# Performance work log

Hardware: AMD Instinct MI355X
Metric: run time of the kernel (lower is better)

The kernel has to match this reference:

```python
import jax, jax.numpy as jnp
import numpy as np

N = 50000      # total nodes
E = 500000     # edges
D = 128        # in_channels
B = 50         # graphs in batch
NPG = N // B   # nodes per graph (equal-sized graphs)
RATIO = 0.5
ALPHA = 0.6


def setup_inputs() -> dict:
    key = jax.random.key(0)
    ks = jax.random.split(key, 8)
    x = jax.random.normal(ks[0], (N, D), dtype=jnp.float32)
    edge_index = jax.random.randint(ks[1], (2, E), 0, N, dtype=jnp.int32)
    batch = jnp.repeat(jnp.arange(B, dtype=jnp.int32), NPG)  # sorted, equal blocks
    s = 1.0 / np.sqrt(D)
    # GCNConv(D,1) for structure score
    W_s = jax.random.normal(ks[2], (D, 1), dtype=jnp.float32) * s
    b_s = jnp.zeros((1,), dtype=jnp.float32)
    # Linear(D,1) for feature score
    W_f = jax.random.normal(ks[3], (1, D), dtype=jnp.float32) * s
    b_f = jnp.zeros((1,), dtype=jnp.float32)
    # GCNConv(D,D) fusion layer
    W_fu = jax.random.normal(ks[4], (D, D), dtype=jnp.float32) * s
    b_fu = jnp.zeros((D,), dtype=jnp.float32)
    return {"x": x, "edge_index": edge_index, "batch": batch,
            "W_s": W_s, "b_s": b_s, "W_f": W_f, "b_f": b_f,
            "W_fu": W_fu, "b_fu": b_fu}


def gcn_conv(x, src, dst, W, b, n):
    """PyG GCNConv: add self loops, symmetric D^-1/2 (A+I) D^-1/2 @ (xW) + b."""
    xw = x @ W                                  # [n, out]
    loop = jnp.arange(n, dtype=src.dtype)
    s = jnp.concatenate([src, loop])
    d = jnp.concatenate([dst, loop])
    deg = jax.ops.segment_sum(jnp.ones_like(s, dtype=xw.dtype), d, num_segments=n)
    dinv = jax.lax.rsqrt(jnp.maximum(deg, 1e-12))
    norm = dinv[s] * dinv[d]                    # [E+n]
    out = jax.ops.segment_sum(norm[:, None] * xw[s], d, num_segments=n)
    return out + b


def reference(x, edge_index, batch, W_s, b_s, W_f, b_f, W_fu, b_fu):
    src, dst = edge_index[0], edge_index[1]
    # fused score: alpha * structure (GCN) + (1-alpha) * feature (Linear)
    score_s = gcn_conv(x, src, dst, W_s, b_s, N)[:, 0]          # [N]
    score_f = (x @ W_f.T + b_f)[:, 0]                           # [N]
    score = jnp.tanh(ALPHA * score_s + (1.0 - ALPHA) * score_f)
    # per-graph top-k (equal-sized graphs -> dense [B, NPG] view, like the torch topk)
    k = int(np.ceil(RATIO * NPG))
    dense = score.reshape(B, NPG)
    order = jnp.argsort(-dense, axis=-1)                        # descending
    offsets = (jnp.arange(B, dtype=jnp.int32) * NPG)[:, None]
    perm = (order[:, :k].astype(jnp.int32) + offsets).reshape(-1)  # [B*k]
    # fusion conv on full graph, then gather selected nodes
    x_fused = gcn_conv(x, src, dst, W_fu, b_fu, N)              # [N, D]
    x_ae = x_fused[perm]                                        # [B*k, D]
    x_out = x_ae * score[perm][:, None]                         # multiplier == 1
    batch_out = batch[perm]
    # filter_adj: remap node ids, keep edges with both endpoints selected
    nodemap = jnp.full((N,), -1, dtype=jnp.int32).at[perm].set(
        jnp.arange(perm.shape[0], dtype=jnp.int32))
    r, c = nodemap[src], nodemap[dst]
    m = (r >= 0) & (c >= 0)
    edge_index_new = jnp.stack([r[m], c[m]], axis=0)
    return (x_out, edge_index_new, batch_out, perm, x_ae)
```

## Files before the change

kernel.cpp:

```cpp
#include <hip/hip_runtime.h>
#include <math.h>

#define N_NODES 50000
#define N_EDGES 500000
#define DIM     128
#define NGRAPH  50
#define NPGC    1000
#define KSEL    500
#define SORT_N  1024
#define NBE     489
#define GEMM_BLKS 782
#define EDGE_BLKS 1954
#define NDINV     196
#define GATH_BLKS 6250
#define DEGB    64
#define NCHUNK  1954


__global__ __launch_bounds__(256) void k1b_deg(const int* __restrict__ dst,
                                               int* __restrict__ degpriv,
                                               int* __restrict__ eslot) {
    int t = threadIdx.x;
    int b = blockIdx.x;
    int* priv = degpriv + b * N_NODES;
    for (int c = b; c < NCHUNK; c += 2 * DEGB) {
        int e1 = (c << 8) + t;
        int cB = c + DEGB;
        int e2 = (cB << 8) + t;
        int d1 = (e1 < N_EDGES) ? dst[e1] : -1;
        int d2 = (cB < NCHUNK && e2 < N_EDGES) ? dst[e2] : -1;
        if (d1 >= 0)
            eslot[e1] = __hip_atomic_fetch_add(&priv[d1], 1, __ATOMIC_RELAXED,
                                               __HIP_MEMORY_SCOPE_WORKGROUP);
        if (d2 >= 0)
            eslot[e2] = __hip_atomic_fetch_add(&priv[d2], 1, __ATOMIC_RELAXED,
                                               __HIP_MEMORY_SCOPE_WORKGROUP);
    }
}


__global__ __launch_bounds__(256) void k1a_gemm_dots(const float* __restrict__ x,
                                                     const float* __restrict__ W,
                                                     float* __restrict__ xw,
                                                     const float* __restrict__ Ws,
                                                     const float* __restrict__ Wf,
                                                     const float* __restrict__ bf,
                                                     double* __restrict__ pack,
                                                     double* __restrict__ sf) {
    __shared__ float lds[12544];
    int t = threadIdx.x;
    float* Wt  = lds;
    float* Xt  = lds + 8192;
    float* Wsl = lds + 12288;
    float* Wfl = lds + 12416;
    int cg = t & 15;
    int ng = t >> 4;
    int node_base = blockIdx.x * 64;

    if (t < 128) Wsl[t] = Ws[t];
    else         Wfl[t - 128] = Wf[t - 128];

    int dn  = t >> 2;
    int dk4 = (t & 3) << 4;
    double ps = 0.0, pf = 0.0;

    float4 acc[4][2];
    #pragma unroll
    for (int nn = 0; nn < 4; nn++) {
        acc[nn][0] = make_float4(0.f, 0.f, 0.f, 0.f);
        acc[nn][1] = make_float4(0.f, 0.f, 0.f, 0.f);
    }
    for (int half = 0; half < 2; half++) {
        const float4* Wg = (const float4*)(W + half * 64 * DIM);
        float4* Wl = (float4*)Wt;
        #pragma unroll
        for (int i = 0; i < 8; i++) {
            int f = t + i * 256;
            Wl[f] = Wg[f];
        }
        #pragma unroll
        for (int i = 0; i < 4; i++) {
            int f = t + i * 256;
            int row = f >> 4, col = f & 15;
            int node = node_base + row;
            float4 v = make_float4(0.f, 0.f, 0.f, 0.f);
            if (node < N_NODES) v = *(const float4*)&x[(size_t)node * DIM + half * 64 + col * 4];
            *(float4*)&Xt[(row << 6) + ((col ^ (row & 15)) << 2)] = v;
        }
        __syncthreads();
        #pragma unroll 2
        for (int kc = 0; kc < 16; kc++) {
            int k = kc << 2;
            float4 wa[4], wb[4];
            #pragma unroll
            for (int kk = 0; kk < 4; kk++) {
                wa[kk] = *(const float4*)&Wt[(k + kk) * DIM + (cg << 2)];
                wb[kk] = *(const float4*)&Wt[(k + kk) * DIM + (cg << 2) + 64];
            }
            int csw = (kc ^ ng) << 2;
            #pragma unroll
            for (int nn = 0; nn < 4; nn++) {
                float4 xv = *(const float4*)&Xt[((ng + (nn << 4)) << 6) + csw];
                acc[nn][0].x += xv.x * wa[0].x + xv.y * wa[1].x + xv.z * wa[2].x + xv.w * wa[3].x;
                acc[nn][0].y += xv.x * wa[0].y + xv.y * wa[1].y + xv.z * wa[2].y + xv.w * wa[3].y;
                acc[nn][0].z += xv.x * wa[0].z + xv.y * wa[1].z + xv.z * wa[2].z + xv.w * wa[3].z;
                acc[nn][0].w += xv.x * wa[0].w + xv.y * wa[1].w + xv.z * wa[2].w + xv.w * wa[3].w;
                acc[nn][1].x += xv.x * wb[0].x + xv.y * wb[1].x + xv.z * wb[2].x + xv.w * wb[3].x;
                acc[nn][1].y += xv.x * wb[0].y + xv.y * wb[1].y + xv.z * wb[2].y + xv.w * wb[3].y;
                acc[nn][1].z += xv.x * wb[0].z + xv.y * wb[1].z + xv.z * wb[2].z + xv.w * wb[3].z;
                acc[nn][1].w += xv.x * wb[0].w + xv.y * wb[1].w + xv.z * wb[2].w + xv.w * wb[3].w;
            }
        }
        #pragma unroll 4
        for (int j = 0; j < 16; j++) {
            int k = dk4 + j;
            int col = k >> 2, sub = k & 3;
            double xd = (double)Xt[(dn << 6) + ((col ^ (dn & 15)) << 2) + sub];
            ps += xd * (double)Wsl[half * 64 + k];
            pf += xd * (double)Wfl[half * 64 + k];
        }
        __syncthreads();
    }
    #pragma unroll
    for (int nn = 0; nn < 4; nn++) {
        int node = node_base + ng + (nn << 4);
        if (node < N_NODES) {
            *(float4*)&xw[(size_t)node * DIM + (cg << 2)]      = acc[nn][0];
            *(float4*)&xw[(size_t)node * DIM + (cg << 2) + 64] = acc[nn][1];
        }
    }
    ps += __shfl_down(ps, 2, 64); ps += __shfl_down(ps, 1, 64);
    pf += __shfl_down(pf, 2, 64); pf += __shfl_down(pf, 1, 64);
    if ((t & 3) == 0) {
        int node = node_base + dn;
        if (node < N_NODES) {
            pack[2 * node + 1] = ps;
            sf[node] = pf + (double)bf[0];
        }
    }
}


__global__ __launch_bounds__(256) void k2_merge(int* __restrict__ degpriv,
                                                int* __restrict__ deg,
                                                int* __restrict__ rowoff,
                                                int* __restrict__ bsums256,
                                                double* __restrict__ pack,
                                                float* __restrict__ dinvf) {
    int t = threadIdx.x;
    int lane = t & 63, wid = t >> 6;
    int i = blockIdx.x * 256 + t;
    int o = 0;
    if (i < N_NODES) {
        #pragma unroll 8
        for (int b = 0; b < DEGB; b++) {
            int* p = &degpriv[b * N_NODES + i];
            int c = *p;
            *p = o;
            o += c;
        }
        deg[i] = o;
        double di = 1.0 / sqrt((double)(o + 1));
        pack[2 * i] = di;
        dinvf[i] = (float)di;
    }
    __shared__ int ws4[4];
    int incl = o;
    #pragma unroll
    for (int off = 1; off < 64; off <<= 1) {
        int u = __shfl_up(incl, off, 64);
        if (lane >= off) incl += u;
    }
    if (lane == 63) ws4[wid] = incl;
    __syncthreads();
    int woff = 0;
    #pragma unroll
    for (int w = 0; w < 4; w++) if (w < wid) woff += ws4[w];
    if (i < N_NODES) rowoff[i] = incl - o + woff;
    if (t == 255) bsums256[blockIdx.x] = woff + incl;
}


__global__ __launch_bounds__(256) void k3_csr(const int* __restrict__ src,
                                              const int* __restrict__ dst,
                                              const int* __restrict__ rowoff,
                                              const int* __restrict__ bsums256,
                                              const int* __restrict__ degpriv,
                                              const int* __restrict__ eslot,
                                              int* __restrict__ csr) {
    __shared__ int bsN[256];
    int t = threadIdx.x;
    if (t < 64) {
        int carry = 0;
        #pragma unroll
        for (int ch = 0; ch < 4; ch++) {
            int i = ch * 64 + t;
            int v = (i < NDINV) ? bsums256[i] : 0;
            int incl = v;
            #pragma unroll
            for (int off = 1; off < 64; off <<= 1) {
                int u = __shfl_up(incl, off, 64);
                if (t >= off) incl += u;
            }
            bsN[i] = incl - v + carry;
            carry += __shfl(incl, 63, 64);
        }
    }
    __syncthreads();
    int e = blockIdx.x * 256 + t;
    if (e >= N_EDGES) return;
    int d = dst[e];
    int owner = (e >> 8) & (DEGB - 1);
    int pos = rowoff[d] + bsN[d >> 8] + degpriv[owner * N_NODES + d] + eslot[e];
    csr[pos] = src[e];
}


__global__ __launch_bounds__(256) void k3b_score(const int* __restrict__ csr,
                                                 const int* __restrict__ rowoff,
                                                 const int* __restrict__ bsums256,
                                                 const int* __restrict__ deg,
                                                 const double* __restrict__ pack,
                                                 double* __restrict__ score_sd) {
    __shared__ int bsN[256];
    int t = threadIdx.x;
    if (t < 64) {
        int carry = 0;
        #pragma unroll
        for (int ch = 0; ch < 4; ch++) {
            int i = ch * 64 + t;
            int v = (i < NDINV) ? bsums256[i] : 0;
            int incl = v;
            #pragma unroll
            for (int off = 1; off < 64; off <<= 1) {
                int u = __shfl_up(incl, off, 64);
                if (t >= off) incl += u;
            }
            bsN[i] = incl - v + carry;
            carry += __shfl(incl, 63, 64);
        }
    }
    __syncthreads();
    int node = blockIdx.x * 256 + t;
    if (node >= N_NODES) return;
    int base = rowoff[node] + bsN[node >> 8];
    int cnt  = deg[node];
    double acc0 = 0.0, acc1 = 0.0;
    int i = 0;
    for (; i + 2 <= cnt; i += 2) {
        int s0 = csr[base + i];
        int s1 = csr[base + i + 1];
        double2 p0 = ((const double2*)pack)[s0];
        double2 p1 = ((const double2*)pack)[s1];
        acc0 += p0.x * p0.y;
        acc1 += p1.x * p1.y;
    }
    if (i < cnt) {
        int s0 = csr[base + i];
        double2 p0 = ((const double2*)pack)[s0];
        acc0 += p0.x * p0.y;
    }
    score_sd[node] = pack[2 * node] * (acc0 + acc1);
}


__global__ __launch_bounds__(512) void k4_topk(const double* __restrict__ score_sd,
                                               const double* __restrict__ pack,
                                               const double* __restrict__ sf,
                                               const float* __restrict__ bs,
                                               const int* __restrict__ batch,
                                               int* __restrict__ perm, int* __restrict__ nodemap,
                                               float* __restrict__ scoref_sel,
                                               float* __restrict__ out, long o2, long o3) {
    __shared__ double key[SORT_N];
    __shared__ int    idx[SORT_N];
    int g = blockIdx.x, t = threadIdx.x;
    const double A = 0.6, OMA = 1.0 - 0.6;
    double bsv = (double)bs[0];
    for (int i = t; i < SORT_N; i += 512) {
        if (i < NPGC) {
            int node = g * NPGC + i;
            double2 p = ((const double2*)pack)[node];
            double tot = score_sd[node] + p.x * p.x * p.y + bsv;
            key[i] = tanh(A * tot + OMA * sf[node]);
            idx[i] = i;
        } else { key[i] = -1e300; idx[i] = i; }
    }
    __syncthreads();
    for (int size = 2; size <= SORT_N; size <<= 1) {
        for (int stride = size >> 1; stride > 0; stride >>= 1) {
            int a = ((t & ~(stride - 1)) << 1) | (t & (stride - 1));
            int b = a | stride;
            bool descFirst = ((a & size) == 0);
            double ka = key[a], kb = key[b];
            int ia = idx[a], ib = idx[b];
            bool aAfterB = (ka < kb) || (ka == kb && ia > ib);
            if (descFirst ? aAfterB : !aAfterB) {
                key[a] = kb; key[b] = ka;
                idx[a] = ib; idx[b] = ia;
            }
            __syncthreads();
        }
    }
    for (int j = t; j < KSEL; j += 512) {
        int node = g * NPGC + idx[j];
        int pos  = g * KSEL + j;
        perm[pos]        = node;
        nodemap[node]    = pos + 1;
        scoref_sel[pos]  = (float)key[j];
        out[o2 + pos]    = (float)batch[node];
        out[o3 + pos]    = (float)node;
    }
}


__global__ __launch_bounds__(256) void k5_escan_gather(const int* __restrict__ src,
                                                       const int* __restrict__ dst,
                                                       const int* __restrict__ nodemap,
                                                       int* __restrict__ epos,
                                                       int* __restrict__ bsumsE,
                                                       const float* __restrict__ xw,
                                                       const int* __restrict__ perm,
                                                       const int* __restrict__ rowoff,
                                                       const int* __restrict__ bsums256,
                                                       const int* __restrict__ deg,
                                                       const int* __restrict__ csr,
                                                       const float* __restrict__ dinvf,
                                                       const float* __restrict__ scoref_sel,
                                                       const float* __restrict__ b_fu,
                                                       float* __restrict__ out, long o4) {
    int t = threadIdx.x;
    int lane = t & 63, wid = t >> 6;
    if (blockIdx.x < NBE) {
        __shared__ int ws4[4];
        int base = blockIdx.x * 1024 + t * 4;
        int v0 = 0, v1 = 0, v2 = 0, v3 = 0;
        if (base + 0 < N_EDGES) v0 = (nodemap[src[base + 0]] > 0 && nodemap[dst[base + 0]] > 0);
        if (base + 1 < N_EDGES) v1 = (nodemap[src[base + 1]] > 0 && nodemap[dst[base + 1]] > 0);
        if (base + 2 < N_EDGES) v2 = (nodemap[src[base + 2]] > 0 && nodemap[dst[base + 2]] > 0);
        if (base + 3 < N_EDGES) v3 = (nodemap[src[base + 3]] > 0 && nodemap[dst[base + 3]] > 0);
        int s4 = v0 + v1 + v2 + v3;
        int incl = s4;
        #pragma unroll
        for (int off = 1; off < 64; off <<= 1) {
            int u = __shfl_up(incl, off, 64);
            if (lane >= off) incl += u;
        }
        if (lane == 63) ws4[wid] = incl;
        __syncthreads();
        int woff = 0;
        #pragma unroll
        for (int w = 0; w < 4; w++) if (w < wid) woff += ws4[w];
        int excl = incl - s4 + woff;
        if (base + 0 < N_EDGES) epos[base + 0] = excl;
        if (base + 1 < N_EDGES) epos[base + 1] = excl + v0;
        if (base + 2 < N_EDGES) epos[base + 2] = excl + v0 + v1;
        if (base + 3 < N_EDGES) epos[base + 3] = excl + v0 + v1 + v2;
        if (t == 255) bsumsE[blockIdx.x] = woff + incl;
        return;
    }
    __shared__ int bsN[256];
    if (t < 64) {
        int carry = 0;
        #pragma unroll
        for (int ch = 0; ch < 4; ch++) {
            int i = ch * 64 + t;
            int v = (i < NDINV) ? bsums256[i] : 0;
            int incl = v;
            #pragma unroll
            for (int off = 1; off < 64; off <<= 1) {
                int u = __shfl_up(incl, off, 64);
                if (t >= off) incl += u;
            }
            bsN[i] = incl - v + carry;
            carry += __shfl(incl, 63, 64);
        }
    }
    __syncthreads();
    int wave = (blockIdx.x - NBE) * 4 + wid;
    int p = perm[wave];
    float dpf = dinvf[p];
    int c2 = lane * 2;
    float2 v = ((const float2*)(xw + (size_t)p * DIM))[lane];
    float nself = dpf * dpf;
    float ax = nself * v.x, ay = nself * v.y;
    int beg = rowoff[p] + bsN[p >> 8], cnt = deg[p];
    int i = 0;
    for (; i + 2 <= cnt; i += 2) {
        int s0 = csr[beg + i];
        int s1 = csr[beg + i + 1];
        float2 u0 = ((const float2*)(xw + (size_t)s0 * DIM))[lane];
        float2 u1 = ((const float2*)(xw + (size_t)s1 * DIM))[lane];
        float n0 = dinvf[s0] * dpf, n1 = dinvf[s1] * dpf;
        ax += n0 * u0.x; ay += n0 * u0.y;
        ax += n1 * u1.x; ay += n1 * u1.y;
    }
    if (i < cnt) {
        int s0 = csr[beg + i];
        float2 u0 = ((const float2*)(xw + (size_t)s0 * DIM))[lane];
        float n0 = dinvf[s0] * dpf;
        ax += n0 * u0.x; ay += n0 * u0.y;
    }
    ax += b_fu[c2];
    ay += b_fu[c2 + 1];
    float sc = scoref_sel[wave];
    size_t ro = (size_t)wave * DIM + c2;
    out[o4 + ro]     = ax;
    out[o4 + ro + 1] = ay;
    out[ro]          = ax * sc;
    out[ro + 1]      = ay * sc;
}


__global__ __launch_bounds__(256) void k6_compact(const int* __restrict__ src,
                                                  const int* __restrict__ dst,
                                                  const int* __restrict__ nodemap,
                                                  const int* __restrict__ epos,
                                                  const int* __restrict__ bsumsE,
                                                  float* __restrict__ out_edges, long M) {
    __shared__ int bsE[512];
    int t = threadIdx.x;
    if (t < 64) {
        int carry = 0;
        #pragma unroll
        for (int c = 0; c < 8; c++) {
            int i = c * 64 + t;
            int v = (i < NBE) ? bsumsE[i] : 0;
            int incl = v;
            #pragma unroll
            for (int off = 1; off < 64; off <<= 1) {
                int u = __shfl_up(incl, off, 64);
                if (t >= off) incl += u;
            }
            if (i < 512) bsE[i] = incl - v + carry;
            carry += __shfl(incl, 63, 64);
        }
    }
    __syncthreads();
    int e = blockIdx.x * 256 + t;
    if (e >= N_EDGES) return;
    int r = nodemap[src[e]], c = nodemap[dst[e]];
    if (r > 0 && c > 0) {
        int pos = epos[e] + bsE[e >> 10];
        out_edges[pos]     = (float)(r - 1);
        out_edges[M + pos] = (float)(c - 1);
    }
}


extern "C" void kernel_launch(void* const* d_in, const int* in_sizes, int n_in,
                              void* d_out, int out_size, void* d_ws, size_t ws_size,
                              hipStream_t stream) {
    const float* x    = (const float*)d_in[0];
    const int*   ei   = (const int*)d_in[1];
    const int*   src  = ei;
    const int*   dst  = ei + N_EDGES;
    const int*   batch= (const int*)d_in[2];
    const float* W_s  = (const float*)d_in[3];
    const float* b_s  = (const float*)d_in[4];
    const float* W_f  = (const float*)d_in[5];
    const float* b_f  = (const float*)d_in[6];
    const float* W_fu = (const float*)d_in[7];
    const float* b_fu = (const float*)d_in[8];
    float* out = (float*)d_out;

    char* wsp = (char*)d_ws;
    size_t off = 0;
    auto take = [&](size_t bytes) -> char* {
        char* p = wsp + off;
        off = (off + bytes + 255) & ~(size_t)255;
        return p;
    };
    char*   zbase      = wsp;
    int*    degpriv    = (int*)   take((size_t)DEGB * N_NODES * 4);
    int*    nodemap    = (int*)   take((size_t)N_NODES * 4);
    size_t  zbytes     = off;
    int*    eslot      = (int*)   take((size_t)N_EDGES * 4);
    int*    deg        = (int*)   take((size_t)N_NODES * 4);
    double* score_sd   = (double*)take((size_t)N_NODES * 8);
    double* pack       = (double*)take((size_t)N_NODES * 16);
    double* sf         = (double*)take((size_t)N_NODES * 8);
    float*  dinvf      = (float*) take((size_t)N_NODES * 4);
    float*  scoref_sel = (float*) take((size_t)NGRAPH * KSEL * 4);
    int*    perm       = (int*)   take((size_t)NGRAPH * KSEL * 4);
    int*    rowoff     = (int*)   take((size_t)N_NODES * 4);
    int*    epos       = (int*)   take((size_t)N_EDGES * 4);
    int*    bsumsE     = (int*)   take((size_t)1024 * 4);
    int*    bsums256   = (int*)   take((size_t)1024 * 4);
    int*    csr        = (int*)   take((size_t)N_EDGES * 4);
    float*  xw         = (float*) take((size_t)N_NODES * DIM * 4);

    long M  = ((long)out_size - 6450000L) / 2;
    long o1 = 3200000L;
    long o2 = o1 + 2 * M;
    long o3 = o2 + (long)NGRAPH * KSEL;
    long o4 = o3 + (long)NGRAPH * KSEL;

    hipMemsetAsync(zbase, 0, zbytes, stream);

    k1b_deg<<<DEGB, 256, 0, stream>>>(dst, degpriv, eslot);
    k1a_gemm_dots<<<GEMM_BLKS, 256, 0, stream>>>(x, W_fu, xw, W_s, W_f, b_f, pack, sf);
    k2_merge<<<NDINV, 256, 0, stream>>>(degpriv, deg, rowoff, bsums256, pack, dinvf);
    k3_csr<<<EDGE_BLKS, 256, 0, stream>>>(src, dst, rowoff, bsums256, degpriv, eslot, csr);
    k3b_score<<<NDINV, 256, 0, stream>>>(csr, rowoff, bsums256, deg, pack, score_sd);
    k4_topk<<<NGRAPH, 512, 0, stream>>>(score_sd, pack, sf, b_s, batch,
                                        perm, nodemap, scoref_sel, out, o2, o3);
    k5_escan_gather<<<NBE + GATH_BLKS, 256, 0, stream>>>(src, dst, nodemap, epos, bsumsE,
                                                         xw, perm, rowoff, bsums256, deg, csr,
                                                         dinvf, scoref_sel, b_fu, out, o4);
    k6_compact<<<EDGE_BLKS, 256, 0, stream>>>(src, dst, nodemap, epos, bsumsE, out + o1, M);
}
```

Before: 233.9 us.

## Fuse degree-count and GEMM kernels into one launch with smaller K tiles

```diff
diff --git a/kernel.cpp b/kernel.cpp
--- a/kernel.cpp
+++ b/kernel.cpp
@@ -17,51 +17,50 @@
 #define NCHUNK  1954
 
 
-__global__ __launch_bounds__(256) void k1b_deg(const int* __restrict__ dst,
-                                               int* __restrict__ degpriv,
-                                               int* __restrict__ eslot) {
+__global__ __launch_bounds__(256) void k1_fused(const float* __restrict__ x,
+                                                const float* __restrict__ W,
+                                                float* __restrict__ xw,
+                                                const float* __restrict__ Ws,
+                                                const float* __restrict__ Wf,
+                                                const float* __restrict__ bf,
+                                                double* __restrict__ pack,
+                                                double* __restrict__ sf,
+                                                const int* __restrict__ dst,
+                                                int* __restrict__ degpriv,
+                                                int* __restrict__ eslot) {
+    __shared__ float lds[6400];
     int t = threadIdx.x;
-    int b = blockIdx.x;
-    int* priv = degpriv + b * N_NODES;
-    for (int c = b; c < NCHUNK; c += 2 * DEGB) {
-        int e1 = (c << 8) + t;
-        int cB = c + DEGB;
-        int e2 = (cB << 8) + t;
-        int d1 = (e1 < N_EDGES) ? dst[e1] : -1;
-        int d2 = (cB < NCHUNK && e2 < N_EDGES) ? dst[e2] : -1;
-        if (d1 >= 0)
-            eslot[e1] = __hip_atomic_fetch_add(&priv[d1], 1, __ATOMIC_RELAXED,
-                                               __HIP_MEMORY_SCOPE_WORKGROUP);
-        if (d2 >= 0)
-            eslot[e2] = __hip_atomic_fetch_add(&priv[d2], 1, __ATOMIC_RELAXED,
-                                               __HIP_MEMORY_SCOPE_WORKGROUP);
-    }
-}
-
-
-__global__ __launch_bounds__(256) void k1a_gemm_dots(const float* __restrict__ x,
-                                                     const float* __restrict__ W,
-                                                     float* __restrict__ xw,
-                                                     const float* __restrict__ Ws,
-                                                     const float* __restrict__ Wf,
-                                                     const float* __restrict__ bf,
-                                                     double* __restrict__ pack,
-                                                     double* __restrict__ sf) {
-    __shared__ float lds[12544];
-    int t = threadIdx.x;
+    if (blockIdx.x < DEGB) {
+        int b = blockIdx.x;
+        int* priv = degpriv + b * N_NODES;
+        for (int c = b; c < NCHUNK; c += 2 * DEGB) {
+            int e1 = (c << 8) + t;
+            int cB = c + DEGB;
+            int e2 = (cB << 8) + t;
+            int d1 = (e1 < N_EDGES) ? dst[e1] : -1;
+            int d2 = (cB < NCHUNK && e2 < N_EDGES) ? dst[e2] : -1;
+            if (d1 >= 0)
+                eslot[e1] = __hip_atomic_fetch_add(&priv[d1], 1, __ATOMIC_RELAXED,
+                                                   __HIP_MEMORY_SCOPE_WORKGROUP);
+            if (d2 >= 0)
+                eslot[e2] = __hip_atomic_fetch_add(&priv[d2], 1, __ATOMIC_RELAXED,
+                                                   __HIP_MEMORY_SCOPE_WORKGROUP);
+        }
+        return;
+    }
     float* Wt  = lds;
-    float* Xt  = lds + 8192;
-    float* Wsl = lds + 12288;
-    float* Wfl = lds + 12416;
+    float* Xt  = lds + 4096;
+    float* Wsl = lds + 6144;
+    float* Wfl = lds + 6272;
     int cg = t & 15;
     int ng = t >> 4;
-    int node_base = blockIdx.x * 64;
+    int node_base = (blockIdx.x - DEGB) * 64;
 
     if (t < 128) Wsl[t] = Ws[t];
     else         Wfl[t - 128] = Wf[t - 128];
 
     int dn  = t >> 2;
-    int dk4 = (t & 3) << 4;
+    int dk8 = (t & 3) << 3;
     double ps = 0.0, pf = 0.0;
 
     float4 acc[4][2];
@@ -70,26 +69,26 @@
         acc[nn][0] = make_float4(0.f, 0.f, 0.f, 0.f);
         acc[nn][1] = make_float4(0.f, 0.f, 0.f, 0.f);
     }
-    for (int half = 0; half < 2; half++) {
-        const float4* Wg = (const float4*)(W + half * 64 * DIM);
+    for (int qtr = 0; qtr < 4; qtr++) {
+        const float4* Wg = (const float4*)W + qtr * 1024;
         float4* Wl = (float4*)Wt;
         #pragma unroll
-        for (int i = 0; i < 8; i++) {
+        for (int i = 0; i < 4; i++) {
             int f = t + i * 256;
             Wl[f] = Wg[f];
         }
         #pragma unroll
-        for (int i = 0; i < 4; i++) {
+        for (int i = 0; i < 2; i++) {
             int f = t + i * 256;
-            int row = f >> 4, col = f & 15;
+            int row = f >> 3, col = f & 7;
             int node = node_base + row;
             float4 v = make_float4(0.f, 0.f, 0.f, 0.f);
-            if (node < N_NODES) v = *(const float4*)&x[(size_t)node * DIM + half * 64 + col * 4];
-            *(float4*)&Xt[(row << 6) + ((col ^ (row & 15)) << 2)] = v;
+            if (node < N_NODES) v = *(const float4*)&x[(size_t)node * DIM + qtr * 32 + col * 4];
+            *(float4*)&Xt[(row << 5) + ((col ^ (row & 7)) << 2)] = v;
         }
         __syncthreads();
         #pragma unroll 2
-        for (int kc = 0; kc < 16; kc++) {
+        for (int kc = 0; kc < 8; kc++) {
             int k = kc << 2;
             float4 wa[4], wb[4];
             #pragma unroll
@@ -97,10 +96,10 @@
                 wa[kk] = *(const float4*)&Wt[(k + kk) * DIM + (cg << 2)];
                 wb[kk] = *(const float4*)&Wt[(k + kk) * DIM + (cg << 2) + 64];
             }
-            int csw = (kc ^ ng) << 2;
+            int csw = (kc ^ (ng & 7)) << 2;
             #pragma unroll
             for (int nn = 0; nn < 4; nn++) {
-                float4 xv = *(const float4*)&Xt[((ng + (nn << 4)) << 6) + csw];
+                float4 xv = *(const float4*)&Xt[((ng + (nn << 4)) << 5) + csw];
                 acc[nn][0].x += xv.x * wa[0].x + xv.y * wa[1].x + xv.z * wa[2].x + xv.w * wa[3].x;
                 acc[nn][0].y += xv.x * wa[0].y + xv.y * wa[1].y + xv.z * wa[2].y + xv.w * wa[3].y;
                 acc[nn][0].z += xv.x * wa[0].z + xv.y * wa[1].z + xv.z * wa[2].z + xv.w * wa[3].z;
@@ -112,12 +111,12 @@
             }
         }
         #pragma unroll 4
-        for (int j = 0; j < 16; j++) {
-            int k = dk4 + j;
-            int col = k >> 2, sub = k & 3;
-            double xd = (double)Xt[(dn << 6) + ((col ^ (dn & 15)) << 2) + sub];
-            ps += xd * (double)Wsl[half * 64 + k];
-            pf += xd * (double)Wfl[half * 64 + k];
+        for (int j = 0; j < 8; j++) {
+            int ko = dk8 + j;
+            int col = ko >> 2, sub = ko & 3;
+            double xd = (double)Xt[(dn << 5) + ((col ^ (dn & 7)) << 2) + sub];
+            ps += xd * (double)Wsl[qtr * 32 + ko];
+            pf += xd * (double)Wfl[qtr * 32 + ko];
         }
         __syncthreads();
     }
@@ -498,8 +497,8 @@
 
     hipMemsetAsync(zbase, 0, zbytes, stream);
 
-    k1b_deg<<<DEGB, 256, 0, stream>>>(dst, degpriv, eslot);
-    k1a_gemm_dots<<<GEMM_BLKS, 256, 0, stream>>>(x, W_fu, xw, W_s, W_f, b_f, pack, sf);
+    k1_fused<<<DEGB + GEMM_BLKS, 256, 0, stream>>>(x, W_fu, xw, W_s, W_f, b_f, pack, sf,
+                                                   dst, degpriv, eslot);
     k2_merge<<<NDINV, 256, 0, stream>>>(degpriv, deg, rowoff, bsums256, pack, dinvf);
     k3_csr<<<EDGE_BLKS, 256, 0, stream>>>(src, dst, rowoff, bsums256, degpriv, eslot, csr);
     k3b_score<<<NDINV, 256, 0, stream>>>(csr, rowoff, bsums256, deg, pack, score_sd);
```

Result: faster. 210.0 us (-10.2%).
